# Performance work log

Hardware: AMD Instinct MI355X
Metric: run time of the kernel (lower is better)

The kernel has to match this reference:

```python
import jax, jax.numpy as jnp
import numpy as np

N = 8192
D_IN = 512
D_OUT = 128
DENSITY = 0.004  # avg degree ~32
NEG_INF = -1.0e10
LEAKY_ALPHA = 0.2  # tf.nn.leaky_relu default


def setup_inputs() -> dict:
    key = jax.random.key(0)
    k_x, k_adj, k_w, k_as, k_an = jax.random.split(key, 5)
    x = jax.random.normal(k_x, (N, D_IN), dtype=jnp.float32)
    # sparse binary adjacency, materialized dense (as the module does via tf.sparse.to_dense)
    adj = (jax.random.uniform(k_adj, (N, N)) < DENSITY).astype(jnp.float32)
    adj = jnp.maximum(adj, jnp.eye(N, dtype=jnp.float32))  # self-loops so softmax rows are valid
    W = jax.random.normal(k_w, (D_IN, D_OUT), dtype=jnp.float32) * (1.0 / np.sqrt(D_IN))
    attn_self = jax.random.normal(k_as, (D_OUT, 1), dtype=jnp.float32) * 0.1
    attn_neigh = jax.random.normal(k_an, (D_OUT, 1), dtype=jnp.float32) * 0.1
    return {"x": x, "adj": adj, "W": W, "attn_self": attn_self, "attn_neigh": attn_neigh}


def reference(x, adj, W, attn_self, attn_neigh):
    # dropouts are 0.0 -> identity
    h = x @ W                                   # [N, D_OUT]
    a_s = h @ attn_self                          # [N, 1]
    a_n = h @ attn_neigh                         # [N, 1]
    e = a_s + a_n.T                              # [N, N] additive attention logits
    e = jnp.where(e >= 0, e, LEAKY_ALPHA * e)    # leaky_relu
    e = e + NEG_INF * (1.0 - adj)                # mask non-edges
    attn = jax.nn.softmax(e, axis=-1)            # row-wise softmax [N, N]
    out = attn @ h                               # [N, D_OUT]
    return jax.nn.relu(out)
```

## Files before the change

kernel.cpp:

```cpp
#include <hip/hip_runtime.h>
#include <hip/hip_bf16.h>
#include <cstdint>

#define NN 8192
#define DIN 512
#define DOUT 128
#define NEG_SLOPE 0.2f
#define MAXE 256
#define GEMM_BLOCKS 1024

typedef float fvec4 __attribute__((ext_vector_type(4)));

__device__ inline fvec4 ntload4(const float* p) {
    return __builtin_nontemporal_load((const fvec4*)p);
}

__global__ __launch_bounds__(256) void k_fused(
    const float* __restrict__ x, const float* __restrict__ W,
    const float* __restrict__ attn_self, const float* __restrict__ attn_neigh,
    const float* __restrict__ adj,
    float* __restrict__ h, float* __restrict__ a_s, float* __restrict__ a_n,
    int* __restrict__ e_cnt, int* __restrict__ e_idx) {
    __shared__ char smem_raw[16384];
    __shared__ int s_cnt;
    const int tid = threadIdx.x;
    const int bid = blockIdx.x;

    if (bid < GEMM_BLOCKS) {
        float4* xs = (float4*)smem_raw;
        const int m0 = bid * 8;
        const float4* x4 = (const float4*)(x + (size_t)m0 * DIN);
#pragma unroll
        for (int r = 0; r < 4; ++r) xs[tid + 256 * r] = x4[tid + 256 * r];
        __syncthreads();

        const int c4 = tid & 31;
        const int rg = tid >> 5;
        const float4* W4 = (const float4*)W;
        const float4* xr = xs + rg * 128;
        float4 acc = {0.f, 0.f, 0.f, 0.f};
#pragma unroll 4
        for (int k4 = 0; k4 < 128; ++k4) {
            float4 xv = xr[k4];
            float4 w0 = W4[(4 * k4 + 0) * 32 + c4];
            float4 w1 = W4[(4 * k4 + 1) * 32 + c4];
            float4 w2 = W4[(4 * k4 + 2) * 32 + c4];
            float4 w3 = W4[(4 * k4 + 3) * 32 + c4];
            acc.x += xv.x * w0.x + xv.y * w1.x + xv.z * w2.x + xv.w * w3.x;
            acc.y += xv.x * w0.y + xv.y * w1.y + xv.z * w2.y + xv.w * w3.y;
            acc.z += xv.x * w0.z + xv.y * w1.z + xv.z * w2.z + xv.w * w3.z;
            acc.w += xv.x * w0.w + xv.y * w1.w + xv.z * w2.w + xv.w * w3.w;
        }
        const int row = m0 + rg;
        ((float4*)h)[(size_t)row * 32 + c4] = acc;

        float4 as4 = ((const float4*)attn_self)[c4];
        float4 an4 = ((const float4*)attn_neigh)[c4];
        float ps = acc.x * as4.x + acc.y * as4.y + acc.z * as4.z + acc.w * as4.w;
        float pn = acc.x * an4.x + acc.y * an4.y + acc.z * an4.z + acc.w * an4.w;
#pragma unroll
        for (int off = 16; off > 0; off >>= 1) {
            ps += __shfl_xor(ps, off);
            pn += __shfl_xor(pn, off);
        }
        if (c4 == 0) { a_s[row] = ps; a_n[row] = pn; }
    } else {
        const int i = bid - GEMM_BLOCKS;
        int* s_idx = (int*)smem_raw;
        if (tid == 0) s_cnt = 0;
        __syncthreads();

        const float* arow = adj + ((size_t)i << 13);
        fvec4 v[8];
#pragma unroll
        for (int r = 0; r < 8; ++r) v[r] = ntload4(arow + 4 * (tid + 256 * r));
#pragma unroll
        for (int r = 0; r < 8; ++r) {
            int base = (tid + 256 * r) * 4;
#pragma unroll
            for (int q = 0; q < 4; ++q) {
                if (v[r][q] != 0.f) {
                    int p = atomicAdd(&s_cnt, 1);
                    if (p < MAXE) s_idx[p] = base + q;
                }
            }
        }
        __syncthreads();
        const int cnt = min(s_cnt, MAXE);
        for (int t = tid; t < cnt; t += 256) e_idx[(size_t)i * MAXE + t] = s_idx[t];
        if (tid == 0) e_cnt[i] = cnt;
    }
}

__global__ __launch_bounds__(256) void k_soft(
    const float* __restrict__ h, const float* __restrict__ a_s,
    const float* __restrict__ a_n, const int* __restrict__ e_cnt,
    const int* __restrict__ e_idx, float* __restrict__ out) {
    const int i = blockIdx.x;
    const int tid = threadIdx.x;
    __shared__ int s_idx[MAXE];
    __shared__ float s_w[MAXE];
    __shared__ float s_red[4];
    __shared__ float s_acc[256];

    const int cnt = e_cnt[i];
    const float asi = a_s[i];

    float lsum = 0.f;
    for (int t = tid; t < cnt; t += 256) {
        int j = e_idx[(size_t)i * MAXE + t];
        s_idx[t] = j;
        float e = asi + a_n[j];
        e = (e >= 0.f) ? e : NEG_SLOPE * e;
        float w = __expf(e);
        s_w[t] = w;
        lsum += w;
    }
#pragma unroll
    for (int off = 32; off > 0; off >>= 1) lsum += __shfl_xor(lsum, off);
    if ((tid & 63) == 0) s_red[tid >> 6] = lsum;
    __syncthreads();
    const float inv_d = 1.0f / (s_red[0] + s_red[1] + s_red[2] + s_red[3]);

    const int c = tid & 127;
    const int half = tid >> 7;
    float acc = 0.f;
    int t = half;
    for (; t + 6 < cnt; t += 8) {
        float w0 = s_w[t];     int j0 = s_idx[t];
        float w1 = s_w[t + 2]; int j1 = s_idx[t + 2];
        float w2 = s_w[t + 4]; int j2 = s_idx[t + 4];
        float w3 = s_w[t + 6]; int j3 = s_idx[t + 6];
        float h0 = h[(size_t)j0 * DOUT + c];
        float h1 = h[(size_t)j1 * DOUT + c];
        float h2 = h[(size_t)j2 * DOUT + c];
        float h3 = h[(size_t)j3 * DOUT + c];
        acc += w0 * h0 + w1 * h1 + w2 * h2 + w3 * h3;
    }
    for (; t < cnt; t += 2) acc += s_w[t] * h[(size_t)s_idx[t] * DOUT + c];

    s_acc[tid] = acc;
    __syncthreads();
    if (tid < 128) {
        float tot = (s_acc[tid] + s_acc[tid + 128]) * inv_d;
        out[(size_t)i * DOUT + tid] = fmaxf(tot, 0.f);
    }
}

extern "C" void kernel_launch(void* const* d_in, const int* in_sizes, int n_in,
                              void* d_out, int out_size, void* d_ws, size_t ws_size,
                              hipStream_t stream) {
    const float* x          = (const float*)d_in[0];
    const float* adj        = (const float*)d_in[1];
    const float* W          = (const float*)d_in[2];
    const float* attn_self  = (const float*)d_in[3];
    const float* attn_neigh = (const float*)d_in[4];
    float* out = (float*)d_out;

    float* h   = (float*)d_ws;
    float* a_s = h + (size_t)NN * DOUT;
    float* a_n = a_s + NN;
    int* e_cnt = (int*)(a_n + NN);
    int* e_idx = e_cnt + NN;

    hipLaunchKernelGGL(k_fused, dim3(GEMM_BLOCKS + NN), dim3(256), 0, stream,
                       x, W, attn_self, attn_neigh, adj, h, a_s, a_n, e_cnt, e_idx);
    hipLaunchKernelGGL(k_soft, dim3(NN), dim3(256), 0, stream,
                       h, a_s, a_n, e_cnt, e_idx, out);
}
```

Before: 416.3 us.

## Process one row per wavefront in softmax-aggregate kernel using shuffles

The aggregation kernel now gives each 64-lane wavefront one node row (four rows per block) instead of one row per 256-thread block. Edge weights and indices are broadcast with wavefront shuffles rather than staged in shared memory, and each lane accumulates two output columns. This removes the block barriers and shared-memory traffic and cuts the grid size by four. The trade-off is less parallelism per row, so high-degree rows are handled serially in chunks of 64.

```diff
diff --git a/kernel.cpp b/kernel.cpp
--- a/kernel.cpp
+++ b/kernel.cpp
@@ -96,55 +96,45 @@
     const float* __restrict__ h, const float* __restrict__ a_s,
     const float* __restrict__ a_n, const int* __restrict__ e_cnt,
     const int* __restrict__ e_idx, float* __restrict__ out) {
-    const int i = blockIdx.x;
     const int tid = threadIdx.x;
-    __shared__ int s_idx[MAXE];
-    __shared__ float s_w[MAXE];
-    __shared__ float s_red[4];
-    __shared__ float s_acc[256];
-
+    const int lane = tid & 63;
+    const int i = blockIdx.x * 4 + (tid >> 6);
     const int cnt = e_cnt[i];
     const float asi = a_s[i];
 
-    float lsum = 0.f;
-    for (int t = tid; t < cnt; t += 256) {
-        int j = e_idx[(size_t)i * MAXE + t];
-        s_idx[t] = j;
-        float e = asi + a_n[j];
-        e = (e >= 0.f) ? e : NEG_SLOPE * e;
-        float w = __expf(e);
-        s_w[t] = w;
+    float acc0 = 0.f, acc1 = 0.f, lsum = 0.f;
+    for (int base = 0; base < cnt; base += 64) {
+        const int len = min(64, cnt - base);
+        int j = 0; float w = 0.f;
+        if (lane < len) {
+            j = e_idx[(size_t)i * MAXE + base + lane];
+            float e = asi + a_n[j];
+            e = (e >= 0.f) ? e : NEG_SLOPE * e;
+            w = __expf(e);
+        }
         lsum += w;
+        int t = 0;
+        for (; t + 1 < len; t += 2) {
+            int jj0 = __shfl(j, t);     float ww0 = __shfl(w, t);
+            int jj1 = __shfl(j, t + 1); float ww1 = __shfl(w, t + 1);
+            float h00 = h[(size_t)jj0 * DOUT + lane];
+            float h01 = h[(size_t)jj0 * DOUT + 64 + lane];
+            float h10 = h[(size_t)jj1 * DOUT + lane];
+            float h11 = h[(size_t)jj1 * DOUT + 64 + lane];
+            acc0 += ww0 * h00 + ww1 * h10;
+            acc1 += ww0 * h01 + ww1 * h11;
+        }
+        if (t < len) {
+            int jj = __shfl(j, t); float ww = __shfl(w, t);
+            acc0 += ww * h[(size_t)jj * DOUT + lane];
+            acc1 += ww * h[(size_t)jj * DOUT + 64 + lane];
+        }
     }
 #pragma unroll
     for (int off = 32; off > 0; off >>= 1) lsum += __shfl_xor(lsum, off);
-    if ((tid & 63) == 0) s_red[tid >> 6] = lsum;
-    __syncthreads();
-    const float inv_d = 1.0f / (s_red[0] + s_red[1] + s_red[2] + s_red[3]);
-
-    const int c = tid & 127;
-    const int half = tid >> 7;
-    float acc = 0.f;
-    int t = half;
-    for (; t + 6 < cnt; t += 8) {
-        float w0 = s_w[t];     int j0 = s_idx[t];
-        float w1 = s_w[t + 2]; int j1 = s_idx[t + 2];
-        float w2 = s_w[t + 4]; int j2 = s_idx[t + 4];
-        float w3 = s_w[t + 6]; int j3 = s_idx[t + 6];
-        float h0 = h[(size_t)j0 * DOUT + c];
-        float h1 = h[(size_t)j1 * DOUT + c];
-        float h2 = h[(size_t)j2 * DOUT + c];
-        float h3 = h[(size_t)j3 * DOUT + c];
-        acc += w0 * h0 + w1 * h1 + w2 * h2 + w3 * h3;
-    }
-    for (; t < cnt; t += 2) acc += s_w[t] * h[(size_t)s_idx[t] * DOUT + c];
-
-    s_acc[tid] = acc;
-    __syncthreads();
-    if (tid < 128) {
-        float tot = (s_acc[tid] + s_acc[tid + 128]) * inv_d;
-        out[(size_t)i * DOUT + tid] = fmaxf(tot, 0.f);
-    }
+    const float inv_d = 1.0f / lsum;
+    out[(size_t)i * DOUT + lane]      = fmaxf(acc0 * inv_d, 0.f);
+    out[(size_t)i * DOUT + 64 + lane] = fmaxf(acc1 * inv_d, 0.f);
 }
 
 extern "C" void kernel_launch(void* const* d_in, const int* in_sizes, int n_in,
@@ -165,6 +155,6 @@
 
     hipLaunchKernelGGL(k_fused, dim3(GEMM_BLOCKS + NN), dim3(256), 0, stream,
                        x, W, attn_self, attn_neigh, adj, h, a_s, a_n, e_cnt, e_idx);
-    hipLaunchKernelGGL(k_soft, dim3(NN), dim3(256), 0, stream,
+    hipLaunchKernelGGL(k_soft, dim3(NN / 4), dim3(256), 0, stream,
                        h, a_s, a_n, e_cnt, e_idx, out);
 }
```

Measured after the change: 407.0 us. -2.2%, faster.
